# Optimization experiments

Measured on AMD Instinct MI355X. Metric: run time of the kernel, lower is better.

## Reference

```python
import jax, jax.numpy as jnp
import numpy as np

B, RES, C = 32, 56, 128
HEADS, WS, NW = 4, 7, 8
HD = C // HEADS            # 32
NQ = NW * NW               # 64 windows
WA = WS * WS               # 49 tokens per window
TOPK = 64


def _topk_closest(q_win, k_win, topk):
    qh, qw = q_win; kh, kw = k_win
    ch_q = np.arange(qh); cw_q = np.arange(qw)
    if qh != kh:
        f = kh // qh
        ch_q = ch_q * f + f // 2
        cw_q = cw_q * f + f // 2
    cq = np.stack(np.meshgrid(ch_q, cw_q, indexing='ij'))              # (2,qh,qw)
    ck = np.stack(np.meshgrid(np.arange(kh), np.arange(kw), indexing='ij'))
    fq = cq.reshape(2, -1); fk = ck.reshape(2, -1)
    rel = fq[:, :, None] - fk[:, None, :]                               # (2,nQ,nK)
    dist = np.sqrt(rel[0].astype(np.float32) ** 2 + rel[1].astype(np.float32) ** 2)
    topk = min(topk, dist.shape[1])
    idx = np.argsort(dist, axis=1, kind='stable')[:, :topk]             # (nQ,topk)
    coord = np.take_along_axis(rel, np.broadcast_to(idx[None], (2,) + idx.shape), axis=2)
    return idx.astype(np.int32), coord.transpose(1, 2, 0).astype(np.float32)


def _buffers():
    # window-relative coords, same as register_buffer('window_coords')
    ch = np.arange(WS) - WS // 2
    wc = np.stack(np.meshgrid(ch, ch, indexing='ij'), axis=-1).reshape(-1, 2).astype(np.float32)  # (49,2)
    # level 0: fine grid (RES x RES); level 1: window grid (NW x NW)
    idx0, c0 = _topk_closest((NW, NW), (RES, RES), TOPK)
    idx1, c1 = _topk_closest((NW, NW), (NW, NW), TOPK)
    c1 = c1 * WS  # k > 0 coords scaled by window size
    coords0 = c0[:, None, :, :] + wc[None, :, None, :]   # (NQ,49,TOPK,2)
    coords1 = c1[:, None, :, :] + wc[None, :, None, :]
    return idx0, idx1, coords0, coords1


def setup_inputs() -> dict:
    key = jax.random.key(0)
    ks = jax.random.split(key, 16)
    idx0, idx1, coords0, coords1 = _buffers()
    s = 0.02
    return {
        'x0': jax.random.normal(ks[0], (B, RES, RES, C), jnp.float32),
        'x1': jax.random.normal(ks[1], (B, NQ, C), jnp.float32),
        'qkv_w': jax.random.normal(ks[2], (3 * C, C), jnp.float32) * s,
        'qkv_b': jnp.zeros((3 * C,), jnp.float32),
        'proj_w': jax.random.normal(ks[3], (C, C), jnp.float32) * s,
        'proj_b': jnp.zeros((C,), jnp.float32),
        'rpb0_w1': jax.random.normal(ks[4], (HD, 2), jnp.float32) * s,
        'rpb0_b1': jnp.zeros((HD,), jnp.float32),
        'rpb0_w2': jax.random.normal(ks[5], (HEADS, HD), jnp.float32) * s,
        'rpb0_b2': jnp.zeros((HEADS,), jnp.float32),
        'rpb1_w1': jax.random.normal(ks[6], (HD, 2), jnp.float32) * s,
        'rpb1_b1': jnp.zeros((HD,), jnp.float32),
        'rpb1_w2': jax.random.normal(ks[7], (HEADS, HD), jnp.float32) * s,
        'rpb1_b2': jnp.zeros((HEADS,), jnp.float32),
        'coords0': jnp.asarray(coords0),
        'coords1': jnp.asarray(coords1),
        'idx0': jnp.asarray(idx0),
        'idx1': jnp.asarray(idx1),
    }


def _rpb_mlp(coords, w1, b1, w2, b2):
    # (NQ,49,T,2) -> (NQ,49,T,heads)
    return jax.nn.relu(coords @ w1.T + b1) @ w2.T + b2


def _gather_kv(kv, idx_flat):
    # kv: (B,L,heads,hd); gathered -> (B,NQ,heads,TOPK,hd)
    g = kv[:, idx_flat]
    return g.reshape(kv.shape[0], NQ, TOPK, HEADS, HD).transpose(0, 1, 3, 2, 4)


def reference(x0, x1, qkv_w, qkv_b, proj_w, proj_b,
              rpb0_w1, rpb0_b1, rpb0_w2, rpb0_b2,
              rpb1_w1, rpb1_b1, rpb1_w2, rpb1_b2,
              coords0, coords1, idx0, idx1):
    b = x0.shape[0]
    scale = HD ** -0.5
    qkv = x0 @ qkv_w.T + qkv_b                       # (B,RES,RES,3C)
    q, k, v = jnp.split(qkv, 3, axis=-1)
    # window-partition q: (B,RES,RES,C) -> (B,NQ,heads,49,hd)
    qw = q.reshape(b, NW, WS, NW, WS, C).transpose(0, 1, 3, 2, 4, 5)
    qw = qw.reshape(b, NQ, WA, HEADS, HD).transpose(0, 1, 3, 2, 4)
    # level 0 KV from fine grid
    k0 = k.reshape(b, RES * RES, HEADS, HD)
    v0 = v.reshape(b, RES * RES, HEADS, HD)
    i0 = idx0.reshape(-1)
    k0s, v0s = _gather_kv(k0, i0), _gather_kv(v0, i0)
    # level 1 KV from pooled tokens (same qkv projection)
    qkv1 = (x1 @ qkv_w.T + qkv_b).reshape(b, NQ, 3, HEADS, HD)
    i1 = idx1.reshape(-1)
    k1s, v1s = _gather_kv(qkv1[:, :, 1], i1), _gather_kv(qkv1[:, :, 2], i1)
    k_all = jnp.concatenate([k0s, k1s], axis=3)      # (B,NQ,heads,2T,hd)
    v_all = jnp.concatenate([v0s, v1s], axis=3)
    attn = jnp.einsum('bqhnd,bqhmd->bqhnm', qw * scale, k_all)  # (B,NQ,heads,49,2T)
    rpb0 = _rpb_mlp(coords0, rpb0_w1, rpb0_b1, rpb0_w2, rpb0_b2)
    rpb1 = _rpb_mlp(coords1, rpb1_w1, rpb1_b1, rpb1_w2, rpb1_b2)
    rpb = jnp.concatenate([rpb0, rpb1], axis=2).transpose(0, 3, 1, 2)  # (NQ,heads,49,2T)
    attn = jax.nn.softmax(attn + rpb[None], axis=-1)
    out = jnp.einsum('bqhnm,bqhmd->bqhnd', attn, v_all)
    out = out.transpose(0, 1, 3, 2, 4).reshape(b * NQ, WA, C)
    return out @ proj_w.T + proj_b
```

## Files before the change

kernel.cpp:

```cpp
#include <hip/hip_runtime.h>
#include <hip/hip_bf16.h>


typedef __bf16 bf16_t;
typedef __bf16 bf16x8 __attribute__((ext_vector_type(8)));
typedef float f32x4 __attribute__((ext_vector_type(4)));

static __device__ __forceinline__ f32x4 mfma_bf16(bf16x8 a, bf16x8 b, f32x4 c) {
  return __builtin_amdgcn_mfma_f32_16x16x32_bf16(a, b, c, 0, 0, 0);
}

static __device__ __forceinline__ bf16x8 cvt8(const float* __restrict__ p) {
  float4 a = *(const float4*)p;
  float4 b = *(const float4*)(p + 4);
  bf16x8 r;
  r[0] = (bf16_t)a.x; r[1] = (bf16_t)a.y; r[2] = (bf16_t)a.z; r[3] = (bf16_t)a.w;
  r[4] = (bf16_t)b.x; r[5] = (bf16_t)b.y; r[6] = (bf16_t)b.z; r[7] = (bf16_t)b.w;
  return r;
}

#define NB 32
#define RES 56
#define CH 128
#define NW 8
#define NQ 64
#define WA 49
#define X0_ROWS (NB * RES * RES)
#define SCALE 0.17677669529663687f
#define SQRT32 5.656854249492381f

__global__ __launch_bounds__(256) void k_qkv(
    const float* __restrict__ x0, const float* __restrict__ x1,
    const float* __restrict__ w, const float* __restrict__ bias,
    bf16_t* __restrict__ qout,
    bf16_t* __restrict__ k0, bf16_t* __restrict__ v0,
    bf16_t* __restrict__ k1, bf16_t* __restrict__ v1) {
  __shared__ __align__(16) bf16_t Asm[64][136];
  __shared__ __align__(16) bf16_t Bsm[128][136];
  const int rb = blockIdx.x;
  const int tid = threadIdx.x;
  const size_t row0 = (size_t)rb * 64;
  const bool is_x0 = (rb < 1568);
  const int b_ = rb / 49;
  const int pix0 = (rb - b_ * 49) * 64;
  const int i1base = (rb - 1568) * 64;

  const float* src = is_x0 ? (x0 + row0 * CH)
                           : (x1 + (row0 - X0_ROWS) * CH);
#pragma unroll
  for (int i = 0; i < 4; ++i) {
    int uid = tid + 256 * i;
    int r = uid >> 4, cs = uid & 15;
    *(bf16x8*)&Asm[r][cs * 8] = cvt8(src + (size_t)r * CH + cs * 8);
  }

  const int wid = tid >> 6, l = tid & 63;
  const int lr = l & 15, lkg = l >> 4, lk = lkg * 8;

  for (int cb = 0; cb < 3; ++cb) {
    const float* wsrc = w + (size_t)cb * 128 * CH;
#pragma unroll
    for (int i = 0; i < 8; ++i) {
      int uid = tid + 256 * i;
      int r = uid >> 4, cs = uid & 15;
      *(bf16x8*)&Bsm[r][cs * 8] = cvt8(wsrc + (size_t)r * CH + cs * 8);
    }
    __syncthreads();

    f32x4 zero = {0.f, 0.f, 0.f, 0.f};
    f32x4 acc[8];
#pragma unroll
    for (int nt = 0; nt < 8; ++nt) acc[nt] = zero;
#pragma unroll
    for (int ks = 0; ks < 4; ++ks) {
      bf16x8 a = *(const bf16x8*)&Asm[wid * 16 + lr][ks * 32 + lk];
#pragma unroll
      for (int nt = 0; nt < 8; ++nt) {
        bf16x8 b = *(const bf16x8*)&Bsm[nt * 16 + lr][ks * 32 + lk];
        acc[nt] = mfma_bf16(a, b, acc[nt]);
      }
    }
    float bias_v[8];
#pragma unroll
    for (int nt = 0; nt < 8; ++nt) bias_v[nt] = bias[cb * 128 + nt * 16 + lr];

#pragma unroll
    for (int r4 = 0; r4 < 4; ++r4) {
      int local = wid * 16 + lkg * 4 + r4;
      if (is_x0) {
        int pix = pix0 + local;
        int rr = pix / 56, cc = pix - rr * 56;
        if (cb == 0) {
          int wn = b_ * 64 + (rr / 7) * 8 + cc / 7;
          int nidx = (rr % 7) * 7 + (cc % 7);
          bf16_t* dst = qout + (size_t)wn * 12544 + nidx * 128;
#pragma unroll
          for (int nt = 0; nt < 8; ++nt)
            dst[nt * 16 + lr] = (bf16_t)(acc[nt][r4] + bias_v[nt]);
        } else {
          bf16_t* dst = (cb == 1 ? k0 : v0) +
                        ((size_t)b_ * 3136 + pix) * CH;
#pragma unroll
          for (int nt = 0; nt < 8; ++nt)
            dst[nt * 16 + lr] = (bf16_t)(acc[nt][r4] + bias_v[nt]);
        }
      } else if (cb != 0) {
        bf16_t* dst = (cb == 1 ? k1 : v1) + (size_t)(i1base + local) * CH;
#pragma unroll
        for (int nt = 0; nt < 8; ++nt)
          dst[nt * 16 + lr] = (bf16_t)(acc[nt][r4] + bias_v[nt]);
      }
    }
    __syncthreads();
  }
}

__global__ __launch_bounds__(256) void k_rpb(
    const float* __restrict__ c0, const float* __restrict__ c1,
    const float* __restrict__ w10, const float* __restrict__ b10,
    const float* __restrict__ w20, const float* __restrict__ b20,
    const float* __restrict__ w11, const float* __restrict__ b11,
    const float* __restrict__ w21, const float* __restrict__ b21,
    float* __restrict__ rpb) {
  __shared__ float w1s[2][32][2], b1s[2][32], w2s[2][4][32], b2s[2][4];
  const int tid = threadIdx.x;
  if (tid < 64) {
    int s = tid >> 5, j = tid & 31;
    const float* w1p = s ? w11 : w10;
    const float* b1p = s ? b11 : b10;
    w1s[s][j][0] = w1p[j * 2];
    w1s[s][j][1] = w1p[j * 2 + 1];
    b1s[s][j] = b1p[j];
  }
  {
    int s = tid >> 7, rem = tid & 127, h = rem >> 5, j = rem & 31;
    w2s[s][h][j] = s ? w21[h * 32 + j] : w20[h * 32 + j];
  }
  if (tid < 8) {
    int s = tid >> 2, h = tid & 3;
    b2s[s][h] = s ? b21[h] : b20[h];
  }
  __syncthreads();

  int L = blockIdx.x * 256 + tid;
  int m = L & 127;
  int n = (L >> 7) % WA;
  int qi = L / (128 * WA);
  int s = m >> 6, mi = m & 63;
  const float* cp = (s ? c1 : c0) + (((size_t)qi * WA + n) * 64 + mi) * 2;
  float cx = cp[0], cy = cp[1];
  float a0 = 0.f, a1 = 0.f, a2 = 0.f, a3 = 0.f;
#pragma unroll
  for (int j = 0; j < 32; ++j) {
    float h = fmaxf(w1s[s][j][0] * cx + w1s[s][j][1] * cy + b1s[s][j], 0.f);
    a0 += w2s[s][0][j] * h;
    a1 += w2s[s][1][j] * h;
    a2 += w2s[s][2][j] * h;
    a3 += w2s[s][3][j] * h;
  }
  size_t base = ((size_t)qi * 4 * WA + n) * 128 + m;
  rpb[base] = (a0 + b2s[s][0]) * SQRT32;
  rpb[base + (size_t)WA * 128] = (a1 + b2s[s][1]) * SQRT32;
  rpb[base + (size_t)2 * WA * 128] = (a2 + b2s[s][2]) * SQRT32;
  rpb[base + (size_t)3 * WA * 128] = (a3 + b2s[s][3]) * SQRT32;
}

__global__ __launch_bounds__(256) void k_attn(
    const bf16_t* qin,
    const bf16_t* __restrict__ k0, const bf16_t* __restrict__ v0,
    const bf16_t* __restrict__ k1, const bf16_t* __restrict__ v1,
    const int* __restrict__ idx0, const int* __restrict__ idx1,
    const float* __restrict__ rpb,
    float* attn_out) {
  __shared__ __align__(16) bf16_t Kt[128][72];
  __shared__ __align__(16) bf16_t Vt[64][136];
  __shared__ __align__(16) bf16_t Sm[64][136];

  const int bid = blockIdx.x;
  const int hp = bid & 1;
  const int qi = (bid >> 1) & 63;
  const int b = bid >> 7;
  const int tid = threadIdx.x;
  const int wn = b * 64 + qi;

#pragma unroll
  for (int i = 0; i < 4; ++i) {
    int uid = tid + 256 * i;
    int key = uid & 127, seg = uid >> 7;
    size_t srcrow;
    const bf16_t *kbase, *vbase;
    if (key < 64) {
      srcrow = (size_t)b * 3136 + idx0[qi * 64 + key];
      kbase = k0; vbase = v0;
    } else {
      srcrow = (size_t)b * 64 + idx1[qi * 64 + key - 64];
      kbase = k1; vbase = v1;
    }
    size_t off = srcrow * CH + hp * 64 + seg * 8;
    *(uint4*)&Kt[key][seg * 8] = *(const uint4*)(kbase + off);
    union { uint4 u; bf16_t h[8]; } cv;
    cv.u = *(const uint4*)(vbase + off);
#pragma unroll
    for (int e = 0; e < 8; ++e) Vt[seg * 8 + e][key] = cv.h[e];
  }

  const int wid = tid >> 6, l = tid & 63;
  const int lr = l & 15, lkg = l >> 4, lk = lkg * 8;
  int qr = wid * 16 + lr;
  if (qr > WA - 1) qr = WA - 1;

  const bf16_t* qb = qin + (size_t)wn * 12544;
  bf16x8 qf[2];
  qf[0] = *(const bf16x8*)&qb[qr * 128 + hp * 64 + lk];
  qf[1] = *(const bf16x8*)&qb[qr * 128 + hp * 64 + 32 + lk];
  __syncthreads();

  const int myrow = wid * 16 + lkg * 4;
  float* obase = attn_out + (size_t)wn * 6272;

#pragma unroll
  for (int lh = 0; lh < 2; ++lh) {
    const int hh = hp * 2 + lh;
    const float* rp = rpb + ((size_t)(qi * 4 + hh) * WA) * 128;
    f32x4 acc[8];
#pragma unroll
    for (int nt = 0; nt < 8; ++nt) {
#pragma unroll
      for (int r4 = 0; r4 < 4; ++r4)
        acc[nt][r4] = rp[(myrow + r4) * 128 + nt * 16 + lr];
    }
#pragma unroll
    for (int nt = 0; nt < 8; ++nt) {
      bf16x8 bfr = *(const bf16x8*)&Kt[nt * 16 + lr][lh * 32 + lk];
      acc[nt] = mfma_bf16(qf[lh], bfr, acc[nt]);
    }
    float mx[4] = {-1e30f, -1e30f, -1e30f, -1e30f};
#pragma unroll
    for (int nt = 0; nt < 8; ++nt)
#pragma unroll
      for (int r4 = 0; r4 < 4; ++r4) mx[r4] = fmaxf(mx[r4], acc[nt][r4]);
#pragma unroll
    for (int m = 1; m < 16; m <<= 1)
#pragma unroll
      for (int r4 = 0; r4 < 4; ++r4)
        mx[r4] = fmaxf(mx[r4], __shfl_xor(mx[r4], m));
    float sum[4] = {0.f, 0.f, 0.f, 0.f};
#pragma unroll
    for (int nt = 0; nt < 8; ++nt)
#pragma unroll
      for (int r4 = 0; r4 < 4; ++r4) {
        float p = __expf(SCALE * (acc[nt][r4] - mx[r4]));
        acc[nt][r4] = p;
        sum[r4] += p;
      }
#pragma unroll
    for (int m = 1; m < 16; m <<= 1)
#pragma unroll
      for (int r4 = 0; r4 < 4; ++r4) sum[r4] += __shfl_xor(sum[r4], m);
#pragma unroll
    for (int nt = 0; nt < 8; ++nt)
#pragma unroll
      for (int r4 = 0; r4 < 4; ++r4)
        Sm[myrow + r4][nt * 16 + lr] = (bf16_t)acc[nt][r4];
    f32x4 zero = {0.f, 0.f, 0.f, 0.f};
    f32x4 oacc[2];
    oacc[0] = zero; oacc[1] = zero;
#pragma unroll
    for (int ks = 0; ks < 4; ++ks) {
      bf16x8 pa = *(const bf16x8*)&Sm[wid * 16 + lr][ks * 32 + lk];
#pragma unroll
      for (int nt2 = 0; nt2 < 2; ++nt2) {
        bf16x8 vb = *(const bf16x8*)&Vt[lh * 32 + nt2 * 16 + lr][ks * 32 + lk];
        oacc[nt2] = mfma_bf16(pa, vb, oacc[nt2]);
      }
    }
#pragma unroll
    for (int nt2 = 0; nt2 < 2; ++nt2)
#pragma unroll
      for (int r4 = 0; r4 < 4; ++r4) {
        int rown = myrow + r4;
        if (rown < WA)
          obase[rown * 128 + hh * 32 + nt2 * 16 + lr] = oacc[nt2][r4] / sum[r4];
      }
  }
}

__global__ __launch_bounds__(256) void k_proj(
    const float* attn,
    const float* __restrict__ pw, const float* __restrict__ pb,
    float* out) {
  __shared__ __align__(16) bf16_t Asm[64][136];
  __shared__ __align__(16) bf16_t Bsm[128][136];
  const int rb = blockIdx.x;
  const int tid = threadIdx.x;
  const size_t row0 = (size_t)rb * 64;
#pragma unroll
  for (int i = 0; i < 4; ++i) {
    int uid = tid + 256 * i;
    int r = uid >> 4, cs = uid & 15;
    *(bf16x8*)&Asm[r][cs * 8] = cvt8(attn + (row0 + r) * CH + cs * 8);
  }
#pragma unroll
  for (int i = 0; i < 8; ++i) {
    int uid = tid + 256 * i;
    int r = uid >> 4, cs = uid & 15;
    *(bf16x8*)&Bsm[r][cs * 8] = cvt8(pw + (size_t)r * CH + cs * 8);
  }
  __syncthreads();

  const int wid = tid >> 6, l = tid & 63;
  const int lr = l & 15, lkg = l >> 4, lk = lkg * 8;
  f32x4 zero = {0.f, 0.f, 0.f, 0.f};
  f32x4 acc[8];
#pragma unroll
  for (int nt = 0; nt < 8; ++nt) acc[nt] = zero;
#pragma unroll
  for (int ks = 0; ks < 4; ++ks) {
    bf16x8 a = *(const bf16x8*)&Asm[wid * 16 + lr][ks * 32 + lk];
#pragma unroll
    for (int nt = 0; nt < 8; ++nt) {
      bf16x8 b = *(const bf16x8*)&Bsm[nt * 16 + lr][ks * 32 + lk];
      acc[nt] = mfma_bf16(a, b, acc[nt]);
    }
  }
#pragma unroll
  for (int nt = 0; nt < 8; ++nt) {
    int n = nt * 16 + lr;
    float bs = pb[n];
#pragma unroll
    for (int r4 = 0; r4 < 4; ++r4) {
      size_t g = row0 + (size_t)(wid * 16 + lkg * 4 + r4);
      out[g * CH + n] = acc[nt][r4] + bs;
    }
  }
}

extern "C" void kernel_launch(void* const* d_in, const int* in_sizes, int n_in,
                              void* d_out, int out_size, void* d_ws, size_t ws_size,
                              hipStream_t stream) {
  const float* x0 = (const float*)d_in[0];
  const float* x1 = (const float*)d_in[1];
  const float* qkv_w = (const float*)d_in[2];
  const float* qkv_b = (const float*)d_in[3];
  const float* proj_w = (const float*)d_in[4];
  const float* proj_b = (const float*)d_in[5];
  const float* rpb0_w1 = (const float*)d_in[6];
  const float* rpb0_b1 = (const float*)d_in[7];
  const float* rpb0_w2 = (const float*)d_in[8];
  const float* rpb0_b2 = (const float*)d_in[9];
  const float* rpb1_w1 = (const float*)d_in[10];
  const float* rpb1_b1 = (const float*)d_in[11];
  const float* rpb1_w2 = (const float*)d_in[12];
  const float* rpb1_b2 = (const float*)d_in[13];
  const float* coords0 = (const float*)d_in[14];
  const float* coords1 = (const float*)d_in[15];
  const int* idx0 = (const int*)d_in[16];
  const int* idx1 = (const int*)d_in[17];

  char* ws = (char*)d_ws;
  bf16_t* k0 = (bf16_t*)(ws + 0);
  bf16_t* v0 = (bf16_t*)(ws + 25690112);
  bf16_t* k1 = (bf16_t*)(ws + 51380224);
  bf16_t* v1 = (bf16_t*)(ws + 51904512);
  float* rpb = (float*)(ws + 52428800);

  k_qkv<<<1600, 256, 0, stream>>>(x0, x1, qkv_w, qkv_b,
                                  (bf16_t*)d_out, k0, v0, k1, v1);
  k_rpb<<<1568, 256, 0, stream>>>(coords0, coords1, rpb0_w1, rpb0_b1, rpb0_w2,
                                  rpb0_b2, rpb1_w1, rpb1_b1, rpb1_w2, rpb1_b2,
                                  rpb);
  k_attn<<<4096, 256, 0, stream>>>((const bf16_t*)d_out, k0, v0, k1, v1,
                                   idx0, idx1, rpb, (float*)d_out);
  k_proj<<<1568, 256, 0, stream>>>((const float*)d_out, proj_w, proj_b,
                                   (float*)d_out);
}
```

Measured before the change: 227.4 us.

## Alias score buffer onto K tile, hoist QK^T for both heads, use exp2/rcp

The attention kernel now computes QK^T for both heads up front, with the bias loads hoisted before the barrier. That frees the K tile, so the softmax probability buffer reuses its LDS instead of a separate array, and a launch bound of 4 blocks per CU is requested. Softmax switches from expf with a subtract to exp2 with a folded scale*log2e FMA, and the division is replaced by a hardware reciprocal. This cuts LDS footprint to raise occupancy, at the cost of more live accumulator registers and an extra barrier.

```diff
diff --git a/kernel.cpp b/kernel.cpp
--- a/kernel.cpp
+++ b/kernel.cpp
@@ -28,6 +28,7 @@
 #define X0_ROWS (NB * RES * RES)
 #define SCALE 0.17677669529663687f
 #define SQRT32 5.656854249492381f
+#define KE 0.25503164508761f
 
 __global__ __launch_bounds__(256) void k_qkv(
     const float* __restrict__ x0, const float* __restrict__ x1,
@@ -165,7 +166,7 @@
   rpb[base + (size_t)3 * WA * 128] = (a3 + b2s[s][3]) * SQRT32;
 }
 
-__global__ __launch_bounds__(256) void k_attn(
+__global__ __launch_bounds__(256, 4) void k_attn(
     const bf16_t* qin,
     const bf16_t* __restrict__ k0, const bf16_t* __restrict__ v0,
     const bf16_t* __restrict__ k1, const bf16_t* __restrict__ v1,
@@ -174,7 +175,7 @@
     float* attn_out) {
   __shared__ __align__(16) bf16_t Kt[128][72];
   __shared__ __align__(16) bf16_t Vt[64][136];
-  __shared__ __align__(16) bf16_t Sm[64][136];
+  bf16_t (*Sm)[136] = (bf16_t(*)[136])&Kt[0][0];
 
   const int bid = blockIdx.x;
   const int hp = bid & 1;
@@ -206,6 +207,7 @@
 
   const int wid = tid >> 6, l = tid & 63;
   const int lr = l & 15, lkg = l >> 4, lk = lkg * 8;
+  const int myrow = wid * 16 + lkg * 4;
   int qr = wid * 16 + lr;
   if (qr > WA - 1) qr = WA - 1;
 
@@ -213,55 +215,69 @@
   bf16x8 qf[2];
   qf[0] = *(const bf16x8*)&qb[qr * 128 + hp * 64 + lk];
   qf[1] = *(const bf16x8*)&qb[qr * 128 + hp * 64 + 32 + lk];
+
+  f32x4 acc[2][8];
+#pragma unroll
+  for (int lh = 0; lh < 2; ++lh) {
+    const float* rp = rpb + ((size_t)(qi * 4 + hp * 2 + lh) * WA) * 128;
+#pragma unroll
+    for (int nt = 0; nt < 8; ++nt)
+#pragma unroll
+      for (int r4 = 0; r4 < 4; ++r4)
+        acc[lh][nt][r4] = rp[(myrow + r4) * 128 + nt * 16 + lr];
+  }
+
   __syncthreads();
 
-  const int myrow = wid * 16 + lkg * 4;
+#pragma unroll
+  for (int lh = 0; lh < 2; ++lh)
+#pragma unroll
+    for (int nt = 0; nt < 8; ++nt) {
+      bf16x8 bfr = *(const bf16x8*)&Kt[nt * 16 + lr][lh * 32 + lk];
+      acc[lh][nt] = mfma_bf16(qf[lh], bfr, acc[lh][nt]);
+    }
+
+  __syncthreads();
+
   float* obase = attn_out + (size_t)wn * 6272;
 
 #pragma unroll
   for (int lh = 0; lh < 2; ++lh) {
     const int hh = hp * 2 + lh;
-    const float* rp = rpb + ((size_t)(qi * 4 + hh) * WA) * 128;
-    f32x4 acc[8];
-#pragma unroll
-    for (int nt = 0; nt < 8; ++nt) {
-#pragma unroll
-      for (int r4 = 0; r4 < 4; ++r4)
-        acc[nt][r4] = rp[(myrow + r4) * 128 + nt * 16 + lr];
-    }
-#pragma unroll
-    for (int nt = 0; nt < 8; ++nt) {
-      bf16x8 bfr = *(const bf16x8*)&Kt[nt * 16 + lr][lh * 32 + lk];
-      acc[nt] = mfma_bf16(qf[lh], bfr, acc[nt]);
-    }
     float mx[4] = {-1e30f, -1e30f, -1e30f, -1e30f};
 #pragma unroll
     for (int nt = 0; nt < 8; ++nt)
 #pragma unroll
-      for (int r4 = 0; r4 < 4; ++r4) mx[r4] = fmaxf(mx[r4], acc[nt][r4]);
+      for (int r4 = 0; r4 < 4; ++r4) mx[r4] = fmaxf(mx[r4], acc[lh][nt][r4]);
 #pragma unroll
     for (int m = 1; m < 16; m <<= 1)
 #pragma unroll
       for (int r4 = 0; r4 < 4; ++r4)
         mx[r4] = fmaxf(mx[r4], __shfl_xor(mx[r4], m));
+    float km[4];
+#pragma unroll
+    for (int r4 = 0; r4 < 4; ++r4) km[r4] = KE * mx[r4];
     float sum[4] = {0.f, 0.f, 0.f, 0.f};
 #pragma unroll
     for (int nt = 0; nt < 8; ++nt)
 #pragma unroll
       for (int r4 = 0; r4 < 4; ++r4) {
-        float p = __expf(SCALE * (acc[nt][r4] - mx[r4]));
-        acc[nt][r4] = p;
+        float p = __builtin_amdgcn_exp2f(fmaf(KE, acc[lh][nt][r4], -km[r4]));
+        acc[lh][nt][r4] = p;
         sum[r4] += p;
       }
 #pragma unroll
     for (int m = 1; m < 16; m <<= 1)
 #pragma unroll
       for (int r4 = 0; r4 < 4; ++r4) sum[r4] += __shfl_xor(sum[r4], m);
+    float inv[4];
+#pragma unroll
+    for (int r4 = 0; r4 < 4; ++r4) inv[r4] = __builtin_amdgcn_rcpf(sum[r4]);
 #pragma unroll
     for (int nt = 0; nt < 8; ++nt)
 #pragma unroll
       for (int r4 = 0; r4 < 4; ++r4)
-        Sm[myrow + r4][nt * 16 + lr] = (bf16_t)acc[nt][r4];
+        Sm[myrow + r4][nt * 16 + lr] = (bf16_t)acc[lh][nt][r4];
     f32x4 zero = {0.f, 0.f, 0.f, 0.f};
     f32x4 oacc[2];
     oacc[0] = zero; oacc[1] = zero;
@@ -280,7 +296,7 @@
       for (int r4 = 0; r4 < 4; ++r4) {
         int rown = myrow + r4;
         if (rown < WA)
-          obase[rown * 128 + hh * 32 + nt2 * 16 + lr] = oacc[nt2][r4] / sum[r4];
+          obase[rown * 128 + hh * 32 + nt2 * 16 + lr] = oacc[nt2][r4] * inv[r4];
       }
   }
 }
```

Result: no change. 227.2 us (-0.1%).
